# Optimization experiments

Measured on AMD Instinct MI355X. Metric: run time of the kernel, lower is better.

## Reference

```python
import jax, jax.numpy as jnp
import numpy as np

K = 8192      # num_codebook_vectors
D = 256       # latent_dim
BETA = 0.25


def setup_inputs() -> dict:
    key = jax.random.key(0)
    k1, k2 = jax.random.split(key)
    z = jax.random.normal(k1, (16, D, 32, 32), dtype=jnp.float32)
    embedding = jax.random.uniform(k2, (K, D), dtype=jnp.float32,
                                   minval=-1.0 / K, maxval=1.0 / K)
    return {"z": z, "embedding": embedding}


def reference(z, embedding):
    # z: (b, d, h, w) -> channels-last (b, h, w, d)
    zp = jnp.transpose(z, (0, 2, 3, 1))
    zf = zp.reshape(-1, D)                                   # (N, D)
    # squared euclidean distances: ||z||^2 + ||e||^2 - 2 z.e
    d = (jnp.sum(zf * zf, axis=1, keepdims=True)
         + jnp.sum(embedding * embedding, axis=1)
         - 2.0 * jnp.matmul(zf, embedding.T))                # (N, K)
    idx = jnp.argmin(d, axis=1)                              # (N,)
    z_q = embedding[idx].reshape(zp.shape)                   # (b, h, w, d)
    sg = jax.lax.stop_gradient
    q_loss = jnp.mean((sg(z_q) - zp) ** 2) + BETA * jnp.mean((z_q - sg(zp)) ** 2)
    # straight-through estimator
    z_q_st = zp + sg(z_q - zp)
    out = jnp.transpose(z_q_st, (0, 3, 1, 2))                # (b, d, h, w)
    return out, q_loss
```

## Files before the change

### kernel.cpp

```cpp
#include <hip/hip_runtime.h>
#include <stdint.h>

#define KCB 8192
#define DDIM 256
#define NROWS 16384
#define NELEM 4194304

typedef __attribute__((ext_vector_type(4))) int   i32x4;
typedef __attribute__((ext_vector_type(8))) int   i32x8;
typedef __attribute__((ext_vector_type(16))) float f32x16;

__device__ __forceinline__ unsigned enc_e2m1(float v) {
    float m = __builtin_fabsf(v);
    unsigned c = 0;
    c += (m >= 0.25f); c += (m >= 0.75f); c += (m >= 1.25f); c += (m >= 1.75f);
    c += (m >= 2.5f);  c += (m >= 3.5f);  c += (m >= 5.0f);
    return c | ((__float_as_uint(v) >> 28) & 8u);
}

__global__ void prep_kernel(const float* __restrict__ z,
                            const float* __restrict__ emb,
                            unsigned char* __restrict__ Ab,
                            unsigned char* __restrict__ Bb,
                            float* __restrict__ zn2p,
                            unsigned* __restrict__ minP,
                            float* __restrict__ loss) {
    int bz = blockIdx.x;
    int t  = threadIdx.x;
    if (bz < 512) {
        int u  = bz * 4 + (t >> 6);
        int L  = t & 63;
        int mb = u >> 2, ks = u & 3;
        int n  = mb * 32 + (L & 31);
        int d0 = ks * 64 + (L >> 5) * 32;
        const float* src = z + (n >> 10) * 262144 + (n & 1023) + d0 * 1024;
        float ss = 0.f;
        unsigned dw[4] = {0u, 0u, 0u, 0u};
        #pragma unroll
        for (int j = 0; j < 32; ++j) {
            float v = src[j * 1024];
            ss += v * v;
            dw[j >> 3] |= enc_e2m1(v) << ((j & 7) * 4);
        }
        zn2p[n * 8 + ks * 2 + (L >> 5)] = ss;
        i32x4 o; o[0] = (int)dw[0]; o[1] = (int)dw[1]; o[2] = (int)dw[2]; o[3] = (int)dw[3];
        *(i32x4*)(Ab + u * 1024 + L * 16) = o;
    } else if (bz < 768) {
        int u  = (bz - 512) * 4 + (t >> 6);
        int L  = t & 63;
        int CB = u >> 3, nf = (u >> 2) & 1, ks = u & 3;
        int n  = CB * 64 + nf * 32 + (L & 31);
        int d0 = ks * 64 + (L >> 5) * 32;
        const float* src = emb + n * DDIM + d0;
        unsigned dw[4] = {0u, 0u, 0u, 0u};
        #pragma unroll
        for (int j = 0; j < 32; ++j) {
            float v = src[j] * 32768.f;
            dw[j >> 3] |= enc_e2m1(v) << ((j & 7) * 4);
        }
        i32x4 o; o[0] = (int)dw[0]; o[1] = (int)dw[1]; o[2] = (int)dw[2]; o[3] = (int)dw[3];
        *(i32x4*)(Bb + u * 1024 + L * 16) = o;
    } else {
        int i = (bz - 768) * 256 + t;
        minP[i] = 0xFFFFFFFFu;
        if (i == 0) *loss = 0.0f;
    }
}

__device__ __forceinline__ i32x8 up8(i32x4 a) {
    i32x8 r;
    r[0] = a[0]; r[1] = a[1]; r[2] = a[2]; r[3] = a[3];
    r[4] = 0; r[5] = 0; r[6] = 0; r[7] = 0;
    return r;
}

__device__ __forceinline__ unsigned umin2(unsigned a, unsigned b) {
    return a < b ? a : b;
}

__global__ __launch_bounds__(512, 2) void gemm_argmin_kernel(
        const unsigned char* __restrict__ Ab, const unsigned char* __restrict__ Bb,
        unsigned* __restrict__ minP) {
    __shared__ unsigned char ldsB[65536];
    int t  = threadIdx.x;
    int bx = blockIdx.x;
    int R2 = bx >> 4;
    int ch = bx & 15;
    int w  = t >> 6, L = t & 63;
    int h  = L >> 5, l31 = L & 31;

    {
        const unsigned char* src = Bb + ch * 65536 + t * 16;
        #pragma unroll
        for (int i = 0; i < 8; ++i)
            __builtin_amdgcn_global_load_lds(
                (const __attribute__((address_space(1))) void*)(src + i * 8192),
                (__attribute__((address_space(3))) void*)(&ldsB[t * 16 + i * 8192]),
                16, 0, 0);
    }

    i32x4 af[2][4];
    #pragma unroll
    for (int mi = 0; mi < 2; ++mi) {
        int mb = R2 * 16 + w * 2 + mi;
        #pragma unroll
        for (int ks = 0; ks < 4; ++ks)
            af[mi][ks] = *(const i32x4*)(Ab + (mb * 4 + ks) * 1024 + L * 16);
    }

    f32x16 zero16;
    #pragma unroll
    for (int r = 0; r < 16; ++r) zero16[r] = 0.f;

    float minpf[32];
    #pragma unroll
    for (int kk = 0; kk < 32; ++kk) minpf[kk] = 3.0e38f;

    __syncthreads();

    for (int nt = 0; nt < 8; ++nt) {
        #pragma unroll
        for (int nh = 0; nh < 2; ++nh) {
            f32x16 acc[2];
            {
                i32x4 b = *(const i32x4*)(&ldsB[(nt * 8 + nh * 4) * 1024 + L * 16]);
                acc[0] = __builtin_amdgcn_mfma_scale_f32_32x32x64_f8f6f4(
                    up8(af[0][0]), up8(b), zero16, 4, 4, 0, 0x7F7F7F7F, 0, 0x7F7F7F7F);
                acc[1] = __builtin_amdgcn_mfma_scale_f32_32x32x64_f8f6f4(
                    up8(af[1][0]), up8(b), zero16, 4, 4, 0, 0x7F7F7F7F, 0, 0x7F7F7F7F);
            }
            #pragma unroll
            for (int ks = 1; ks < 4; ++ks) {
                i32x4 b = *(const i32x4*)(&ldsB[(nt * 8 + nh * 4 + ks) * 1024 + L * 16]);
                acc[0] = __builtin_amdgcn_mfma_scale_f32_32x32x64_f8f6f4(
                    up8(af[0][ks]), up8(b), acc[0], 4, 4, 0, 0x7F7F7F7F, 0, 0x7F7F7F7F);
                acc[1] = __builtin_amdgcn_mfma_scale_f32_32x32x64_f8f6f4(
                    up8(af[1][ks]), up8(b), acc[1], 4, 4, 0, 0x7F7F7F7F, 0, 0x7F7F7F7F);
            }
            const float C = (float)(8388608 + nt * 2 + nh);
            #pragma unroll
            for (int mi = 0; mi < 2; ++mi)
                #pragma unroll
                for (int r = 0; r < 16; ++r) {
                    float k = fmaf(acc[mi][r], -16384.0f, C);
                    int kk = mi * 16 + r;
                    minpf[kk] = fminf(minpf[kk], k);
                }
        }
    }

    unsigned minp32[32];
    {
        unsigned colbase = (unsigned)(ch * 512 + l31);
        #pragma unroll
        for (int kk = 0; kk < 32; ++kk) {
            unsigned v    = (unsigned)minpf[kk];
            unsigned colc = v & 15u;
            unsigned col  = colbase + (colc << 5);
            minp32[kk] = ((v - colc) << 1) | col;
        }
    }

    #pragma unroll
    for (int ml = 1; ml <= 16; ml <<= 1)
        #pragma unroll
        for (int kk = 0; kk < 32; ++kk) {
            unsigned o = __shfl_xor(minp32[kk], ml);
            minp32[kk] = umin2(minp32[kk], o);
        }
    if (l31 == 0) {
        #pragma unroll
        for (int kk = 0; kk < 32; ++kk) {
            int mi = kk >> 4, reg = kk & 15;
            int row = R2 * 512 + w * 64 + mi * 32
                    + (reg & 3) + 8 * (reg >> 2) + 4 * h;
            atomicMin(&minP[row], minp32[kk]);
        }
    }
}

__global__ void finalize_kernel(const float* __restrict__ emb,
                                const float* __restrict__ zn2p,
                                const unsigned* __restrict__ minP,
                                float* __restrict__ out,
                                float* __restrict__ loss) {
    __shared__ float ez[32 * 257];
    __shared__ int   idxs[32];
    __shared__ float wsum[4];
    int t  = threadIdx.x;
    int bh = blockIdx.x;
    float rterm = 0.f;
    if (t < 32) {
        int n = bh * 32 + t;
        unsigned key = minP[n];
        idxs[t] = (int)(key & 0x1FFFu);
        float acc = fmaf((float)(key >> 13), -0.25f, 512.0f);
        float4 p0 = *(const float4*)(zn2p + n * 8);
        float4 p1 = *(const float4*)(zn2p + n * 8 + 4);
        float zn2 = p0.x + p0.y + p0.z + p0.w + p1.x + p1.y + p1.z + p1.w;
        rterm = zn2 - acc * 6.103515625e-5f;
    }
    __syncthreads();
    {
        int f = t & 63, rl = t >> 6;
        #pragma unroll
        for (int i = 0; i < 8; ++i) {
            int wl  = rl + i * 4;
            int idx = idxs[wl];
            float4 v = *(const float4*)(emb + idx * DDIM + f * 4);
            float* dst = &ez[wl * 257 + f * 4];
            dst[0] = v.x; dst[1] = v.y; dst[2] = v.z; dst[3] = v.w;
        }
    }
    __syncthreads();
    int wq = t & 31;
    int dg = t >> 5;
    int off0 = (bh >> 5) * 262144 + (bh & 31) * 32 + wq;
    const float* ezrow = &ez[wq * 257];
    float lacc = rterm;
    #pragma unroll
    for (int it = 0; it < 32; ++it) {
        int d = it * 8 + dg;
        float zq = ezrow[d];
        out[off0 + d * 1024] = zq;
        lacc += zq * zq;
    }
    #pragma unroll
    for (int ml = 1; ml <= 32; ml <<= 1) lacc += __shfl_xor(lacc, ml);
    if ((t & 63) == 0) wsum[t >> 6] = lacc;
    __syncthreads();
    if (t == 0) {
        float tot = wsum[0] + wsum[1] + wsum[2] + wsum[3];
        atomicAdd(loss, tot * (1.25f / (float)NELEM));
    }
}

extern "C" void kernel_launch(void* const* d_in, const int* in_sizes, int n_in,
                              void* d_out, int out_size, void* d_ws, size_t ws_size,
                              hipStream_t stream) {
    const float* z   = (const float*)d_in[0];
    const float* emb = (const float*)d_in[1];
    float* out  = (float*)d_out;
    float* loss = out + NELEM;

    char* ws = (char*)d_ws;
    unsigned* minP = (unsigned*)ws;
    float* zn2p = (float*)(ws + 65536);
    unsigned char* Ab = (unsigned char*)d_out;
    unsigned char* Bb = Ab + (size_t)NROWS * DDIM / 2;

    hipLaunchKernelGGL(prep_kernel,        dim3(832), dim3(256), 0, stream,
                       z, emb, Ab, Bb, zn2p, minP, loss);
    hipLaunchKernelGGL(gemm_argmin_kernel, dim3(512), dim3(512), 0, stream,
                       Ab, Bb, minP);
    hipLaunchKernelGGL(finalize_kernel,    dim3(512), dim3(256), 0, stream,
                       emb, zn2p, minP, out, loss);
}
```

Before: 115.3 us.

## Fuse finalize into GEMM-argmin via last-block-per-row-group counter

Removes the separate finalize kernel launch. Each of the 16 blocks covering a 512-row group atomically bumps a counter, and the last one to finish gathers the codebook rows, writes the output and adds its part of the loss. The packed FP4 operands move from the output buffer into the workspace so the fused epilogue cannot overwrite them. This saves one launch and its tail gap, but the finalize work now runs on only 32 blocks (one per row group) instead of 512, which risks serialising the epilogue.

```diff
diff --git a/kernel.cpp b/kernel.cpp
--- a/kernel.cpp
+++ b/kernel.cpp
@@ -24,6 +24,7 @@
                             unsigned char* __restrict__ Bb,
                             float* __restrict__ zn2p,
                             unsigned* __restrict__ minP,
+                            unsigned* __restrict__ cnt,
                             float* __restrict__ loss) {
     int bz = blockIdx.x;
     int t  = threadIdx.x;
@@ -63,6 +64,7 @@
     } else {
         int i = (bz - 768) * 256 + t;
         minP[i] = 0xFFFFFFFFu;
+        if (bz == 768 && t < 32) cnt[t] = 0u;
         if (i == 0) *loss = 0.0f;
     }
 }
@@ -80,8 +82,11 @@
 
 __global__ __launch_bounds__(512, 2) void gemm_argmin_kernel(
         const unsigned char* __restrict__ Ab, const unsigned char* __restrict__ Bb,
-        unsigned* __restrict__ minP) {
-    __shared__ unsigned char ldsB[65536];
+        unsigned* __restrict__ minP, unsigned* __restrict__ cnt,
+        const float* __restrict__ emb, const float* __restrict__ zn2p,
+        float* __restrict__ out, float* __restrict__ loss) {
+    __shared__ __align__(16) unsigned char smem[65536];
+    unsigned char* ldsB = smem;
     int t  = threadIdx.x;
     int bx = blockIdx.x;
     int R2 = bx >> 4;
@@ -177,60 +182,64 @@
             atomicMin(&minP[row], minp32[kk]);
         }
     }
-}
-
-__global__ void finalize_kernel(const float* __restrict__ emb,
-                                const float* __restrict__ zn2p,
-                                const unsigned* __restrict__ minP,
-                                float* __restrict__ out,
-                                float* __restrict__ loss) {
-    __shared__ float ez[32 * 257];
-    __shared__ int   idxs[32];
-    __shared__ float wsum[4];
-    int t  = threadIdx.x;
-    int bh = blockIdx.x;
-    float rterm = 0.f;
-    if (t < 32) {
-        int n = bh * 32 + t;
-        unsigned key = minP[n];
-        idxs[t] = (int)(key & 0x1FFFu);
-        float acc = fmaf((float)(key >> 13), -0.25f, 512.0f);
-        float4 p0 = *(const float4*)(zn2p + n * 8);
-        float4 p1 = *(const float4*)(zn2p + n * 8 + 4);
-        float zn2 = p0.x + p0.y + p0.z + p0.w + p1.x + p1.y + p1.z + p1.w;
-        rterm = zn2 - acc * 6.103515625e-5f;
-    }
-    __syncthreads();
-    {
-        int f = t & 63, rl = t >> 6;
-        #pragma unroll
-        for (int i = 0; i < 8; ++i) {
-            int wl  = rl + i * 4;
+
+    __threadfence();
+    int* sflag = (int*)(smem + 33056);
+    if (t == 0) sflag[0] = (atomicAdd(&cnt[R2], 1u) == 15u) ? 1 : 0;
+    __syncthreads();
+    if (!sflag[0]) return;
+
+    __threadfence();
+    float* ez   = (float*)smem;
+    int*   idxs = (int*)(smem + 32896);
+    float* wsum = (float*)(smem + 33024);
+    int f4  = t & 63;
+    int r8  = t >> 6;
+    int wq  = t & 31;
+    int dgr = t >> 5;
+    float lacc = 0.f;
+    for (int it = 0; it < 16; ++it) {
+        int bh = R2 * 16 + it;
+        __syncthreads();
+        if (t < 32) {
+            int n = bh * 32 + t;
+            unsigned key = minP[n];
+            idxs[t] = (int)(key & 0x1FFFu);
+            float a2 = fmaf((float)(key >> 13), -0.25f, 512.0f);
+            float4 p0 = *(const float4*)(zn2p + n * 8);
+            float4 p1 = *(const float4*)(zn2p + n * 8 + 4);
+            float zn2 = p0.x + p0.y + p0.z + p0.w + p1.x + p1.y + p1.z + p1.w;
+            lacc += zn2 - a2 * 6.103515625e-5f;
+        }
+        __syncthreads();
+        #pragma unroll
+        for (int i = 0; i < 4; ++i) {
+            int wl  = r8 + i * 8;
             int idx = idxs[wl];
-            float4 v = *(const float4*)(emb + idx * DDIM + f * 4);
-            float* dst = &ez[wl * 257 + f * 4];
+            float4 v = *(const float4*)(emb + idx * DDIM + f4 * 4);
+            float* dst = &ez[wl * 257 + f4 * 4];
             dst[0] = v.x; dst[1] = v.y; dst[2] = v.z; dst[3] = v.w;
         }
-    }
-    __syncthreads();
-    int wq = t & 31;
-    int dg = t >> 5;
-    int off0 = (bh >> 5) * 262144 + (bh & 31) * 32 + wq;
-    const float* ezrow = &ez[wq * 257];
-    float lacc = rterm;
-    #pragma unroll
-    for (int it = 0; it < 32; ++it) {
-        int d = it * 8 + dg;
-        float zq = ezrow[d];
-        out[off0 + d * 1024] = zq;
-        lacc += zq * zq;
+        __syncthreads();
+        int off0 = (bh >> 5) * 262144 + (bh & 31) * 32 + wq;
+        const float* ezrow = &ez[wq * 257];
+        #pragma unroll
+        for (int j = 0; j < 16; ++j) {
+            int d = j * 16 + dgr;
+            float zq = ezrow[d];
+            out[off0 + d * 1024] = zq;
+            lacc += zq * zq;
+        }
     }
     #pragma unroll
     for (int ml = 1; ml <= 32; ml <<= 1) lacc += __shfl_xor(lacc, ml);
+    __syncthreads();
     if ((t & 63) == 0) wsum[t >> 6] = lacc;
     __syncthreads();
     if (t == 0) {
-        float tot = wsum[0] + wsum[1] + wsum[2] + wsum[3];
+        float tot = 0.f;
+        #pragma unroll
+        for (int q = 0; q < 8; ++q) tot += wsum[q];
         atomicAdd(loss, tot * (1.25f / (float)NELEM));
     }
 }
@@ -246,13 +255,12 @@
     char* ws = (char*)d_ws;
     unsigned* minP = (unsigned*)ws;
     float* zn2p = (float*)(ws + 65536);
-    unsigned char* Ab = (unsigned char*)d_out;
-    unsigned char* Bb = Ab + (size_t)NROWS * DDIM / 2;
+    unsigned* cnt = (unsigned*)(ws + 589824);
+    unsigned char* Ab = (unsigned char*)ws + (1 << 20);
+    unsigned char* Bb = Ab + 2 * 1024 * 1024;
 
     hipLaunchKernelGGL(prep_kernel,        dim3(832), dim3(256), 0, stream,
-                       z, emb, Ab, Bb, zn2p, minP, loss);
+                       z, emb, Ab, Bb, zn2p, minP, cnt, loss);
     hipLaunchKernelGGL(gemm_argmin_kernel, dim3(512), dim3(512), 0, stream,
-                       Ab, Bb, minP);
-    hipLaunchKernelGGL(finalize_kernel,    dim3(512), dim3(256), 0, stream,
-                       emb, zn2p, minP, out, loss);
-}
+                       Ab, Bb, minP, cnt, emb, zn2p, out, loss);
+}
```

Result: slower. 230.0 us (+99.5%).
